# Performance work log

Measured on AMD Instinct MI355X. Metric: run time of the kernel, lower is better.

Reference implementation:

```python
import jax, jax.numpy as jnp
import numpy as np

BATCH = 64          # number of sequences
K = 4               # speculative tokens per sequence (uniform)
VOCAB = 128000


def setup_inputs() -> dict:
    key = jax.random.key(0)
    k1, k2 = jax.random.split(key)
    # total rows = BATCH * (K + 1): one bonus token per sequence
    logits = jax.random.normal(k1, (BATCH * (K + 1), VOCAB), dtype=jnp.float32)
    spec_token_ids = jax.random.randint(k2, (BATCH, K), 0, VOCAB, dtype=jnp.int32)
    return {"logits": logits, "spec_token_ids": spec_token_ids}


def reference(logits, spec_token_ids):
    """Greedy rejection sampling for speculative decoding.

    logits: [B*(K+1), V] -- target-model logits for K spec tokens + 1 bonus
    spec_token_ids: [B, K] int -- draft tokens
    Returns [B, K+1] int32 token ids, padded with -1 after the first rejection
    (equivalent to the ragged Python lists of the original, -1 = absent).
    """
    B, Kk = spec_token_ids.shape
    # [B, K+1] greedy tokens from the target model
    out_ids = jnp.argmax(logits, axis=-1).astype(jnp.int32).reshape(B, Kk + 1)
    # accept spec token i only if all tokens 0..i matched
    match = (spec_token_ids == out_ids[:, :Kk]).astype(jnp.int32)       # [B, K]
    accepted_prefix = jnp.cumprod(match, axis=1)                         # [B, K]
    # number of emitted tokens = accepted spec tokens + 1 (correction/bonus)
    num_emitted = accepted_prefix.sum(axis=1) + 1                        # [B]
    pos = jnp.arange(Kk + 1, dtype=jnp.int32)                            # [K+1]
    return jnp.where(pos[None, :] < num_emitted[:, None], out_ids, -1)
```

## Files before the change

### kernel.cpp

```cpp
#include <hip/hip_runtime.h>

#define BATCH 64
#define KSPEC 4
#define ROWS (BATCH * (KSPEC + 1))
#define VOCAB 128000

__global__ __launch_bounds__(1024) void argmax_rows_kernel(
    const float* __restrict__ logits, int* __restrict__ row_argmax) {
    const int row = blockIdx.x;
    const int tid = threadIdx.x;
    const float4* rowp = (const float4*)(logits + (long long)row * VOCAB);
    const int nvec = VOCAB / 4;

    float best = -__builtin_inff();
    int bidx = 0x7fffffff;

    for (int i = tid; i < nvec; i += 1024) {
        float4 v = rowp[i];
        int base = i * 4;
        if (v.x > best || (v.x == best && base     < bidx)) { best = v.x; bidx = base;     }
        if (v.y > best || (v.y == best && base + 1 < bidx)) { best = v.y; bidx = base + 1; }
        if (v.z > best || (v.z == best && base + 2 < bidx)) { best = v.z; bidx = base + 2; }
        if (v.w > best || (v.w == best && base + 3 < bidx)) { best = v.w; bidx = base + 3; }
    }

    #pragma unroll
    for (int off = 32; off > 0; off >>= 1) {
        float ov = __shfl_down(best, off, 64);
        int   oi = __shfl_down(bidx, off, 64);
        if (ov > best || (ov == best && oi < bidx)) { best = ov; bidx = oi; }
    }

    __shared__ float svals[16];
    __shared__ int   sidx[16];
    const int wave = tid >> 6;
    const int lane = tid & 63;
    if (lane == 0) { svals[wave] = best; sidx[wave] = bidx; }
    __syncthreads();

    if (wave == 0) {
        best = (lane < 16) ? svals[lane] : -__builtin_inff();
        bidx = (lane < 16) ? sidx[lane]  : 0x7fffffff;
        #pragma unroll
        for (int off = 8; off > 0; off >>= 1) {
            float ov = __shfl_down(best, off, 64);
            int   oi = __shfl_down(bidx, off, 64);
            if (ov > best || (ov == best && oi < bidx)) { best = ov; bidx = oi; }
        }
        if (lane == 0) row_argmax[row] = bidx;
    }
}

__global__ void accept_kernel(const int* __restrict__ row_argmax,
                              const int* __restrict__ spec_ids,
                              int* __restrict__ out) {
    const int b = threadIdx.x;
    if (b >= BATCH) return;
    const int* ids = row_argmax + b * (KSPEC + 1);

    int num = 1;
    bool ok = true;
    #pragma unroll
    for (int i = 0; i < KSPEC; i++) {
        ok = ok && (spec_ids[b * KSPEC + i] == ids[i]);
        if (ok) num++;
    }
    #pragma unroll
    for (int i = 0; i <= KSPEC; i++) {
        out[b * (KSPEC + 1) + i] = (i < num) ? ids[i] : -1;
    }
}

extern "C" void kernel_launch(void* const* d_in, const int* in_sizes, int n_in,
                              void* d_out, int out_size, void* d_ws, size_t ws_size,
                              hipStream_t stream) {
    const float* logits  = (const float*)d_in[0];
    const int* spec_ids  = (const int*)d_in[1];
    int* out             = (int*)d_out;
    int* row_argmax      = (int*)d_ws;

    argmax_rows_kernel<<<ROWS, 1024, 0, stream>>>(logits, row_argmax);
    accept_kernel<<<1, 64, 0, stream>>>(row_argmax, spec_ids, out);
}
```

Baseline: 234.4 us.

## Split each row argmax across segment blocks with packed 64-bit keys

```diff
diff --git a/kernel.cpp b/kernel.cpp
--- a/kernel.cpp
+++ b/kernel.cpp
@@ -4,81 +4,95 @@
 #define KSPEC 4
 #define ROWS (BATCH * (KSPEC + 1))
 #define VOCAB 128000
+#define NVEC  (VOCAB / 4)
+#define SEGS  8
+#define SEGV  (NVEC / SEGS)
 
-__global__ __launch_bounds__(1024) void argmax_rows_kernel(
-    const float* __restrict__ logits, int* __restrict__ row_argmax) {
-    const int row = blockIdx.x;
+__device__ __forceinline__ unsigned long long make_key(float f, int idx) {
+    unsigned int u = __float_as_uint(f);
+    u ^= ((unsigned int)((int)u >> 31)) | 0x80000000u;
+    return ((unsigned long long)u << 32) | (unsigned int)(~idx);
+}
+
+__device__ __forceinline__ unsigned long long umax64(unsigned long long a,
+                                                     unsigned long long b) {
+    return a > b ? a : b;
+}
+
+__global__ __launch_bounds__(256) void argmax_partial_kernel(
+    const float* __restrict__ logits, unsigned long long* __restrict__ partials) {
+    const int blk = blockIdx.x;
+    const int row = blk >> 3;
+    const int seg = blk & (SEGS - 1);
     const int tid = threadIdx.x;
-    const float4* rowp = (const float4*)(logits + (long long)row * VOCAB);
-    const int nvec = VOCAB / 4;
 
-    float best = -__builtin_inff();
-    int bidx = 0x7fffffff;
+    const float4* p = (const float4*)(logits + (long long)row * VOCAB) + seg * SEGV;
+    const int base = seg * SEGV * 4;
 
-    for (int i = tid; i < nvec; i += 1024) {
-        float4 v = rowp[i];
-        int base = i * 4;
-        if (v.x > best || (v.x == best && base     < bidx)) { best = v.x; bidx = base;     }
-        if (v.y > best || (v.y == best && base + 1 < bidx)) { best = v.y; bidx = base + 1; }
-        if (v.z > best || (v.z == best && base + 2 < bidx)) { best = v.z; bidx = base + 2; }
-        if (v.w > best || (v.w == best && base + 3 < bidx)) { best = v.w; bidx = base + 3; }
+    unsigned long long best = 0ull;
+    for (int i = tid; i < SEGV; i += 256) {
+        float4 v = p[i];
+        int idx = base + i * 4;
+        best = umax64(best, make_key(v.x, idx));
+        best = umax64(best, make_key(v.y, idx + 1));
+        best = umax64(best, make_key(v.z, idx + 2));
+        best = umax64(best, make_key(v.w, idx + 3));
     }
 
     #pragma unroll
-    for (int off = 32; off > 0; off >>= 1) {
-        float ov = __shfl_down(best, off, 64);
-        int   oi = __shfl_down(bidx, off, 64);
-        if (ov > best || (ov == best && oi < bidx)) { best = ov; bidx = oi; }
-    }
+    for (int off = 32; off > 0; off >>= 1)
+        best = umax64(best, __shfl_down(best, off, 64));
 
-    __shared__ float svals[16];
-    __shared__ int   sidx[16];
+    __shared__ unsigned long long sk[4];
     const int wave = tid >> 6;
     const int lane = tid & 63;
-    if (lane == 0) { svals[wave] = best; sidx[wave] = bidx; }
+    if (lane == 0) sk[wave] = best;
     __syncthreads();
 
-    if (wave == 0) {
-        best = (lane < 16) ? svals[lane] : -__builtin_inff();
-        bidx = (lane < 16) ? sidx[lane]  : 0x7fffffff;
-        #pragma unroll
-        for (int off = 8; off > 0; off >>= 1) {
-            float ov = __shfl_down(best, off, 64);
-            int   oi = __shfl_down(bidx, off, 64);
-            if (ov > best || (ov == best && oi < bidx)) { best = ov; bidx = oi; }
-        }
-        if (lane == 0) row_argmax[row] = bidx;
+    if (tid == 0) {
+        best = umax64(umax64(sk[0], sk[1]), umax64(sk[2], sk[3]));
+        partials[blk] = best;
     }
 }
 
-__global__ void accept_kernel(const int* __restrict__ row_argmax,
-                              const int* __restrict__ spec_ids,
-                              int* __restrict__ out) {
-    const int b = threadIdx.x;
-    if (b >= BATCH) return;
-    const int* ids = row_argmax + b * (KSPEC + 1);
+__global__ void finalize_kernel(const unsigned long long* __restrict__ partials,
+                                const int* __restrict__ spec_ids,
+                                int* __restrict__ out) {
+    __shared__ int sidx[ROWS];
+    const int t = threadIdx.x;
 
-    int num = 1;
-    bool ok = true;
-    #pragma unroll
-    for (int i = 0; i < KSPEC; i++) {
-        ok = ok && (spec_ids[b * KSPEC + i] == ids[i]);
-        if (ok) num++;
+    if (t < ROWS) {
+        unsigned long long best = partials[t * SEGS];
+        #pragma unroll
+        for (int j = 1; j < SEGS; j++)
+            best = umax64(best, partials[t * SEGS + j]);
+        sidx[t] = (int)(~(unsigned int)best);
     }
-    #pragma unroll
-    for (int i = 0; i <= KSPEC; i++) {
-        out[b * (KSPEC + 1) + i] = (i < num) ? ids[i] : -1;
+    __syncthreads();
+
+    if (t < BATCH) {
+        const int* ids = sidx + t * (KSPEC + 1);
+        int num = 1;
+        bool ok = true;
+        #pragma unroll
+        for (int i = 0; i < KSPEC; i++) {
+            ok = ok && (spec_ids[t * KSPEC + i] == ids[i]);
+            if (ok) num++;
+        }
+        #pragma unroll
+        for (int i = 0; i <= KSPEC; i++)
+            out[t * (KSPEC + 1) + i] = (i < num) ? ids[i] : -1;
     }
 }
 
 extern "C" void kernel_launch(void* const* d_in, const int* in_sizes, int n_in,
                               void* d_out, int out_size, void* d_ws, size_t ws_size,
                               hipStream_t stream) {
-    const float* logits  = (const float*)d_in[0];
-    const int* spec_ids  = (const int*)d_in[1];
-    int* out             = (int*)d_out;
-    int* row_argmax      = (int*)d_ws;
+    const float* logits = (const float*)d_in[0];
+    const int* spec_ids = (const int*)d_in[1];
+    int* out            = (int*)d_out;
+    unsigned long long* partials = (unsigned long long*)d_ws;
 
-    argmax_rows_kernel<<<ROWS, 1024, 0, stream>>>(logits, row_argmax);
-    accept_kernel<<<1, 64, 0, stream>>>(row_argmax, spec_ids, out);
+    argmax_partial_kernel<<<ROWS * SEGS, 256, 0, stream>>>(logits, partials);
+    finalize_kernel<<<1, 384, 0, stream>>>(partials, spec_ids, out);
 }
```

Result: no change. 232.2 us (-0.9%).
